# Performance work log

Measured on AMD Instinct MI355X. Metric: run time of the kernel, lower is better.

## Reference

```python
import jax, jax.numpy as jnp
import numpy as np

N, E, FIN, H, C = 100000, 1600000, 128, 64, 40
EPS = 1e-5

def setup_inputs() -> dict:
    key = jax.random.key(0)
    ks = jax.random.split(key, 20)
    inp = {
        'x': jax.random.normal(ks[0], (N, FIN), jnp.float32),
        'edge_idx': jax.random.randint(ks[1], (2, E), 0, N, dtype=jnp.int64),
        'W1': jax.random.normal(ks[2], (FIN, H), jnp.float32) / np.sqrt(FIN),
        'b1': jnp.zeros((H,), jnp.float32),
        'g1': jnp.ones((H,), jnp.float32),
        'be1': jnp.zeros((H,), jnp.float32),
        'm1': jax.random.normal(ks[3], (H,), jnp.float32) * 0.1,
        'v1': jax.random.uniform(ks[4], (H,), jnp.float32) + 0.5,
        'W2': jax.random.normal(ks[5], (H, H), jnp.float32) / np.sqrt(H),
        'b2': jnp.zeros((H,), jnp.float32),
        'g2': jnp.ones((H,), jnp.float32),
        'be2': jnp.zeros((H,), jnp.float32),
        'm2': jax.random.normal(ks[6], (H,), jnp.float32) * 0.1,
        'v2': jax.random.uniform(ks[7], (H,), jnp.float32) + 0.5,
        'W3': jax.random.normal(ks[8], (H, C), jnp.float32) / np.sqrt(H),
        'b3': jnp.zeros((C,), jnp.float32),
    }
    return inp

def reference(x, edge_idx, W1, b1, g1, be1, m1, v1, W2, b2, g2, be2, m2, v2, W3, b3):
    n = x.shape[0]
    loop = jnp.arange(n, dtype=edge_idx.dtype)
    row = jnp.concatenate([edge_idx[0], loop])  # source nodes (+ self loops)
    col = jnp.concatenate([edge_idx[1], loop])  # target nodes (+ self loops)
    # symmetric gcn_norm: deg from unit edge weights aggregated at target
    deg = jax.ops.segment_sum(jnp.ones_like(row, dtype=x.dtype), col, num_segments=n)
    dinv = jnp.where(deg > 0, jax.lax.rsqrt(deg), 0.0)
    norm = dinv[row] * dinv[col]  # [E+N]

    def conv(h, W, b):
        hl = h @ W                            # dense transform first (PyG order)
        msg = hl[row] * norm[:, None]         # gather + edge scale
        agg = jax.ops.segment_sum(msg, col, num_segments=n)  # scatter-add
        return agg + b

    def bn(h, g, be, m, v):  # eval-mode BatchNorm1d (running stats)
        return g * (h - m) * jax.lax.rsqrt(v + EPS) + be

    h = jax.nn.relu(bn(conv(x, W1, b1), g1, be1, m1, v1))
    h = jax.nn.relu(bn(conv(h, W2, b2), g2, be2, m2, v2))
    return conv(h, W3, b3)
```

## Files before the change

### kernel.cpp

```cpp
#include <hip/hip_runtime.h>

#define EPSV 1e-5f
#define NB  1024
#define CAP 2048
#define BIN_ITER 4

typedef short short8 __attribute__((ext_vector_type(8)));
typedef float f32x4 __attribute__((ext_vector_type(4)));

__device__ inline unsigned short f2bf(float x) {
    unsigned u = __float_as_uint(x);
    unsigned r = (u + 0x7FFFu + ((u >> 16) & 1u)) >> 16;
    return (unsigned short)r;
}
__device__ inline float bf2f(unsigned short h) {
    return __uint_as_float(((unsigned)h) << 16);
}
__device__ inline float bflo(unsigned u) { return __uint_as_float(u << 16); }
__device__ inline float bfhi(unsigned u) { return __uint_as_float(u & 0xffff0000u); }
__device__ inline unsigned packbf(float x, float y) {
    return (unsigned)f2bf(x) | ((unsigned)f2bf(y) << 16);
}


__global__ __launch_bounds__(1024) void k_bin(const int* __restrict__ row,
                                              const int* __restrict__ col,
                                              int* __restrict__ bcnt,
                                              unsigned* __restrict__ bkt,
                                              int E, int npb) {
    __shared__ int hist[NB];
    __shared__ int fill[NB];
    const int tid = threadIdx.x;
    const int e0 = blockIdx.x * (1024 * BIN_ITER);
    for (int j = tid; j < NB; j += 1024) hist[j] = 0;
    __syncthreads();
    unsigned ent[BIN_ITER];
    int bb[BIN_ITER];
#pragma unroll
    for (int j = 0; j < BIN_ITER; ++j) {
        const int i = e0 + j * 1024 + tid;
        bb[j] = -1;
        ent[j] = 0;
        if (i < E) {
            const int c = col[i], r = row[i];
            const int b = c / npb;
            bb[j] = b;
            ent[j] = ((unsigned)(c - b * npb) << 17) | (unsigned)r;
            atomicAdd(&hist[b], 1);
        }
    }
    __syncthreads();
    for (int j = tid; j < NB; j += 1024)
        fill[j] = hist[j] ? atomicAdd(&bcnt[j], hist[j]) : 0;
    __syncthreads();
#pragma unroll
    for (int j = 0; j < BIN_ITER; ++j) {
        if (bb[j] >= 0) {
            const int pos = atomicAdd(&fill[bb[j]], 1);
            if (pos < CAP)
                bkt[(size_t)bb[j] * CAP + pos] = ent[j];
        }
    }
}


__global__ __launch_bounds__(NB) void k_bscan(const int* __restrict__ bcnt,
                                              int* __restrict__ bbase,
                                              int* __restrict__ rowptr, int E, int n) {
    __shared__ int s[NB];
    const int t = threadIdx.x;
    const int v = min(bcnt[t], CAP);
    s[t] = v;
    __syncthreads();
    for (int off = 1; off < NB; off <<= 1) {
        int u = (t >= off) ? s[t - off] : 0;
        __syncthreads();
        s[t] += u;
        __syncthreads();
    }
    bbase[t] = s[t] - v;
    if (t == 0) rowptr[n] = E;
}


__global__ __launch_bounds__(256) void k_place(const int* __restrict__ bcnt,
                                               const int* __restrict__ bbase,
                                               const unsigned* __restrict__ bkt,
                                               int* __restrict__ rowptr,
                                               float* __restrict__ dinv,
                                               int* __restrict__ srcidx,
                                               int n, int npb) {
    __shared__ int hist[128];
    __shared__ int pfx[128];
    __shared__ unsigned ent[CAP];
    const int b = blockIdx.x;
    const int tid = threadIdx.x;
    const int c0 = b * npb;
    const int nn = min(npb, n - c0);
    if (nn <= 0) return;
    const int bc = min(bcnt[b], CAP);
    const int base = bbase[b];
    for (int j = tid; j < nn; j += 256) hist[j] = 0;
    __syncthreads();
    for (int i = tid; i < bc; i += 256) {
        const unsigned e = bkt[(size_t)b * CAP + i];
        ent[i] = e;
        atomicAdd(&hist[e >> 17], 1);
    }
    __syncthreads();
    if (tid == 0) {
        int run = base;
        for (int j = 0; j < nn; ++j) { pfx[j] = run; run += hist[j]; }
    }
    __syncthreads();
    for (int j = tid; j < nn; j += 256) {
        rowptr[c0 + j] = pfx[j];
        dinv[c0 + j] = rsqrtf((float)(hist[j] + 1));
    }
    __syncthreads();
    for (int i = tid; i < bc; i += 256) {
        const unsigned e = ent[i];
        const int pos = atomicAdd(&pfx[e >> 17], 1);
        srcidx[pos] = (int)(e & 0x1FFFFu);
    }
}


template<int K, int F, int NT>
__device__ inline void wprep_one(const float* __restrict__ W,
                                 unsigned short* __restrict__ out, int tid) {
    const int lane = tid & 63;
    const int nt = (tid >> 6) % NT;
    const int ks = tid / (64 * NT);
    const int col = nt * 16 + (lane & 15);
    const int k0 = ks * 32 + (lane >> 4) * 8;
    short8 h8, l8;
#pragma unroll
    for (int e = 0; e < 8; ++e) {
        const float w = (col < F) ? W[(size_t)(k0 + e) * F + col] : 0.f;
        const unsigned short h = f2bf(w);
        h8[e] = (short)h;
        l8[e] = (short)f2bf(w - bf2f(h));
    }
    short8* dst = (short8*)(out + (size_t)tid * 16);
    dst[0] = h8;
    dst[1] = l8;
}

__global__ __launch_bounds__(256) void k_wprep_all(const float* __restrict__ W1,
                                                   const float* __restrict__ W2,
                                                   const float* __restrict__ W3,
                                                   unsigned short* __restrict__ wf1,
                                                   unsigned short* __restrict__ wf2,
                                                   unsigned short* __restrict__ wf3) {
    const int tid = blockIdx.x * blockDim.x + threadIdx.x;
    if (tid < 1024) wprep_one<128, 64, 4>(W1, wf1, tid);
    else if (tid < 1536) wprep_one<64, 64, 4>(W2, wf2, tid - 1024);
    else if (tid < 1920) wprep_one<64, 40, 3>(W3, wf3, tid - 1536);
}


template<int K, int NT>
__global__ __launch_bounds__(256) void gemm_f32in(const float* __restrict__ X,
                                                  const unsigned short* __restrict__ wfrag,
                                                  const float* __restrict__ dinv,
                                                  unsigned* __restrict__ Y, int n) {
    const int lane = threadIdx.x & 63;
    const int wv = threadIdx.x >> 6;
    const int row0 = blockIdx.x * 64 + wv * 16;
    const int arow = row0 + (lane & 15);
    const bool aval = arow < n;

    f32x4 acc[NT];
#pragma unroll
    for (int t = 0; t < NT; ++t) acc[t] = (f32x4){0.f, 0.f, 0.f, 0.f};

#pragma unroll
    for (int ks = 0; ks < K / 32; ++ks) {
        float av[8];
        if (aval) {
            const float* ap = X + (size_t)arow * K + ks * 32 + (lane >> 4) * 8;
            const float4 p0 = *reinterpret_cast<const float4*>(ap);
            const float4 p1 = *reinterpret_cast<const float4*>(ap + 4);
            av[0] = p0.x; av[1] = p0.y; av[2] = p0.z; av[3] = p0.w;
            av[4] = p1.x; av[5] = p1.y; av[6] = p1.z; av[7] = p1.w;
        } else {
#pragma unroll
            for (int e = 0; e < 8; ++e) av[e] = 0.f;
        }
        short8 ah, al;
#pragma unroll
        for (int e = 0; e < 8; ++e) {
            const unsigned short h = f2bf(av[e]);
            ah[e] = (short)h;
            al[e] = (short)f2bf(av[e] - bf2f(h));
        }
#pragma unroll
        for (int t = 0; t < NT; ++t) {
            const short8* bp = (const short8*)(wfrag + (((size_t)ks * NT + t) * 64 + lane) * 16);
            const short8 bh = bp[0];
            const short8 bl = bp[1];
            acc[t] = __builtin_amdgcn_mfma_f32_16x16x32_bf16(ah, bh, acc[t], 0, 0, 0);
            acc[t] = __builtin_amdgcn_mfma_f32_16x16x32_bf16(al, bh, acc[t], 0, 0, 0);
            acc[t] = __builtin_amdgcn_mfma_f32_16x16x32_bf16(ah, bl, acc[t], 0, 0, 0);
        }
    }

    const int col = lane & 15;
    const int rg = lane >> 4;
#pragma unroll
    for (int r = 0; r < 4; ++r) {
        const int orow = row0 + rg * 4 + r;
        const float di = (orow < n) ? dinv[orow] : 0.f;
#pragma unroll
        for (int t = 0; t < NT; ++t) {
            const float val = acc[t][r] * di;
            const float oth = __shfl_xor(val, 1);
            if (!(lane & 1))
                Y[(size_t)orow * (NT * 8) + t * 8 + (col >> 1)] = packbf(val, oth);
        }
    }
}


template<int K, int NT, int MODE>
__global__ __launch_bounds__(256) void gemm_bf16in(const unsigned short* __restrict__ X,
                                                   const unsigned short* __restrict__ wfrag,
                                                   const float* __restrict__ dinv,
                                                   const float* __restrict__ bias,
                                                   void* __restrict__ Yv, int n) {
    const int lane = threadIdx.x & 63;
    const int wv = threadIdx.x >> 6;
    const int row0 = blockIdx.x * 64 + wv * 16;
    const int arow = row0 + (lane & 15);
    const bool aval = arow < n;

    f32x4 acc[NT];
#pragma unroll
    for (int t = 0; t < NT; ++t) acc[t] = (f32x4){0.f, 0.f, 0.f, 0.f};

#pragma unroll
    for (int ks = 0; ks < K / 32; ++ks) {
        short8 ah = {0, 0, 0, 0, 0, 0, 0, 0};
        if (aval)
            ah = *(const short8*)(X + (size_t)arow * K + ks * 32 + (lane >> 4) * 8);
#pragma unroll
        for (int t = 0; t < NT; ++t) {
            const short8* bp = (const short8*)(wfrag + (((size_t)ks * NT + t) * 64 + lane) * 16);
            const short8 bh = bp[0];
            const short8 bl = bp[1];
            acc[t] = __builtin_amdgcn_mfma_f32_16x16x32_bf16(ah, bh, acc[t], 0, 0, 0);
            acc[t] = __builtin_amdgcn_mfma_f32_16x16x32_bf16(ah, bl, acc[t], 0, 0, 0);
        }
    }

    const int col = lane & 15;
    const int rg = lane >> 4;
#pragma unroll
    for (int r = 0; r < 4; ++r) {
        const int orow = row0 + rg * 4 + r;
        if (MODE == 0) {
            const float di = (orow < n) ? dinv[orow] : 0.f;
            unsigned* Y = (unsigned*)Yv;
#pragma unroll
            for (int t = 0; t < NT; ++t) {
                const float val = acc[t][r] * di;
                const float oth = __shfl_xor(val, 1);
                if (!(lane & 1))
                    Y[(size_t)orow * (NT * 8) + t * 8 + (col >> 1)] = packbf(val, oth);
            }
        } else {
            float* Y = (float*)Yv;
#pragma unroll
            for (int t = 0; t < NT; ++t) {
                const int oc = t * 16 + col;
                if (orow < n && oc < 40)
                    Y[(size_t)orow * 40 + oc] = acc[t][r] + bias[oc];
            }
        }
    }
}


template<int MODE>
__global__ __launch_bounds__(256) void k_gather(const unsigned* __restrict__ in,
                                                const int* __restrict__ rowptr,
                                                const int* __restrict__ srcidx,
                                                const float* __restrict__ dinv,
                                                const float* __restrict__ b,
                                                const float* __restrict__ g,
                                                const float* __restrict__ be,
                                                const float* __restrict__ m,
                                                const float* __restrict__ v,
                                                unsigned* __restrict__ out, int n) {
    __shared__ unsigned offs[4][64];
    const int lane = threadIdx.x & 63;
    const int wslot = threadIdx.x >> 6;
    const int half = lane >> 5;
    const int p = lane & 31;
    const int node = blockIdx.x * 4 + wslot;

    if (node >= n) {
        if (!half) out[(size_t)node * 32 + p] = 0u;
        return;
    }

    const int s = rowptr[node], e = rowptr[node + 1];
    const unsigned pconst = (unsigned)p * 4u;
    const char* inb = (const char*)in;
    float ax = 0.f, ay = 0.f;

    for (int base = s; base < e; base += 64) {
        const int c = min(64, e - base);
        unsigned idx = (unsigned)n;
        if (base + lane < e) idx = (unsigned)srcidx[base + lane];
        offs[wslot][lane] = idx * 128u;
        for (int k8 = 0; k8 < 32; k8 += 8) {
            if (2 * k8 >= c) break;
            unsigned o[8], u[8];
#pragma unroll
            for (int j = 0; j < 8; ++j) o[j] = offs[wslot][2 * (k8 + j) + half];
#pragma unroll
            for (int j = 0; j < 8; ++j)
                u[j] = *(const unsigned*)(inb + (size_t)(o[j] + pconst));
#pragma unroll
            for (int j = 0; j < 8; ++j) { ax += bflo(u[j]); ay += bfhi(u[j]); }
        }
    }
    ax += __shfl_xor(ax, 32);
    ay += __shfl_xor(ay, 32);
    {
        const unsigned su = in[(size_t)node * 32 + p];
        ax += bflo(su); ay += bfhi(su);
    }
    const float di = dinv[node];
    float ox, oy;
    if (MODE == 2) {
        ox = ax * di; oy = ay * di;
    } else {
        const float2 bb = ((const float2*)b)[p];
        const float2 gg = ((const float2*)g)[p];
        const float2 bee = ((const float2*)be)[p];
        const float2 mm = ((const float2*)m)[p];
        const float2 vv = ((const float2*)v)[p];
        const float sx = gg.x * rsqrtf(vv.x + EPSV);
        const float sy = gg.y * rsqrtf(vv.y + EPSV);
        ox = fmaxf((ax * di + bb.x - mm.x) * sx + bee.x, 0.f);
        oy = fmaxf((ay * di + bb.y - mm.y) * sy + bee.y, 0.f);
        if (MODE == 1) { ox *= di; oy *= di; }
    }
    if (!half) out[(size_t)node * 32 + p] = packbf(ox, oy);
}


extern "C" void kernel_launch(void* const* d_in, const int* in_sizes, int n_in,
                              void* d_out, int out_size, void* d_ws, size_t ws_size,
                              hipStream_t stream) {
    const float* x   = (const float*)d_in[0];
    const int*   ei  = (const int*)d_in[1];
    const float* W1  = (const float*)d_in[2];
    const float* b1  = (const float*)d_in[3];
    const float* g1  = (const float*)d_in[4];
    const float* be1 = (const float*)d_in[5];
    const float* m1  = (const float*)d_in[6];
    const float* v1  = (const float*)d_in[7];
    const float* W2  = (const float*)d_in[8];
    const float* b2  = (const float*)d_in[9];
    const float* g2  = (const float*)d_in[10];
    const float* be2 = (const float*)d_in[11];
    const float* m2  = (const float*)d_in[12];
    const float* v2  = (const float*)d_in[13];
    const float* W3  = (const float*)d_in[14];
    const float* b3  = (const float*)d_in[15];

    const int n = in_sizes[0] / 128;
    const int E = in_sizes[1] / 2;
    const int* row  = ei;
    const int* colv = ei + E;
    const int npb = (n + NB - 1) / NB;
    const int gblk = (n >> 6) + 1;
    const int npad = gblk * 64;

    char* base = (char*)d_ws;
    size_t off = 0;
    auto alloc = [&](size_t bytes) -> char* {
        char* p = base + off;
        off += (bytes + 255) & ~(size_t)255;
        return p;
    };
    int*      bcnt   = (int*)     alloc((size_t)NB * 4);
    int*      bbase  = (int*)     alloc((size_t)NB * 4);
    unsigned* bkt    = (unsigned*)alloc((size_t)NB * CAP * 4);
    int*      rowptr = (int*)     alloc((size_t)(n + 1) * 4);
    int*      srcidx = (int*)     alloc((size_t)E * 4);
    float*    dinv   = (float*)   alloc((size_t)n * 4);
    unsigned* hls1u  = (unsigned*)alloc((size_t)npad * 32 * 4);
    unsigned* h1u    = (unsigned*)alloc((size_t)npad * 32 * 4);
    unsigned* hls2u  = (unsigned*)alloc((size_t)npad * 32 * 4);
    unsigned* h2lsu  = (unsigned*)alloc((size_t)npad * 32 * 4);
    unsigned* agg3u  = (unsigned*)alloc((size_t)npad * 32 * 4);
    unsigned short* wf1 = (unsigned short*)alloc((size_t)(128/32) * 4 * 64 * 32);
    unsigned short* wf2 = (unsigned short*)alloc((size_t)(64/32) * 4 * 64 * 32);
    unsigned short* wf3 = (unsigned short*)alloc((size_t)(64/32) * 3 * 64 * 32);
    float*    outp   = (float*)d_out;

    hipMemsetAsync(bcnt, 0, (size_t)NB * 4, stream);
    const int binblk = (E + 1024 * BIN_ITER - 1) / (1024 * BIN_ITER);
    k_bin<<<binblk, 1024, 0, stream>>>(row, colv, bcnt, bkt, E, npb);
    k_bscan<<<1, NB, 0, stream>>>(bcnt, bbase, rowptr, E, n);
    k_place<<<NB, 256, 0, stream>>>(bcnt, bbase, bkt, rowptr, dinv, srcidx, n, npb);

    k_wprep_all<<<8, 256, 0, stream>>>(W1, W2, W3, wf1, wf2, wf3);

    const int ablk = npad / 4;
    gemm_f32in<128, 4><<<gblk, 256, 0, stream>>>(x, wf1, dinv, hls1u, n);
    k_gather<0><<<ablk, 256, 0, stream>>>(hls1u, rowptr, srcidx, dinv,
                                          b1, g1, be1, m1, v1, h1u, n);
    gemm_bf16in<64, 4, 0><<<gblk, 256, 0, stream>>>((const unsigned short*)h1u, wf2,
                                                    dinv, nullptr, hls2u, n);
    k_gather<1><<<ablk, 256, 0, stream>>>(hls2u, rowptr, srcidx, dinv,
                                          b2, g2, be2, m2, v2, h2lsu, n);
    k_gather<2><<<ablk, 256, 0, stream>>>(h2lsu, rowptr, srcidx, dinv,
                                          nullptr, nullptr, nullptr, nullptr, nullptr,
                                          agg3u, n);
    gemm_bf16in<64, 3, 1><<<gblk, 256, 0, stream>>>((const unsigned short*)agg3u, wf3,
                                                    dinv, b3, outp, n);
}
```

Measured before the change: 196.0 us.

## Process eight nodes per wavefront in CSR gather, drop LDS index staging

The gather kernel now assigns eight consecutive nodes to each wavefront instead of one. Row pointers are loaded once per wave and broadcast with readlane, and the BatchNorm parameters are hoisted out of the per-node loop. Neighbor indices are read directly from global memory in groups of 16 rather than staged through shared memory, which removes LDS traffic and per-node launch overhead. The cost is fewer waves in flight for latency hiding, and the 16-edge granularity wastes lanes on low-degree nodes.

Measured after the change: 201.9 us. 3.0% more time.

```diff
diff --git a/kernel.cpp b/kernel.cpp
--- a/kernel.cpp
+++ b/kernel.cpp
@@ -292,64 +292,71 @@
                                                 const float* __restrict__ be,
                                                 const float* __restrict__ m,
                                                 const float* __restrict__ v,
-                                                unsigned* __restrict__ out, int n) {
-    __shared__ unsigned offs[4][64];
+                                                unsigned* __restrict__ out,
+                                                int n, int E) {
     const int lane = threadIdx.x & 63;
-    const int wslot = threadIdx.x >> 6;
     const int half = lane >> 5;
     const int p = lane & 31;
-    const int node = blockIdx.x * 4 + wslot;
-
-    if (node >= n) {
-        if (!half) out[(size_t)node * 32 + p] = 0u;
-        return;
-    }
-
-    const int s = rowptr[node], e = rowptr[node + 1];
-    const unsigned pconst = (unsigned)p * 4u;
-    const char* inb = (const char*)in;
-    float ax = 0.f, ay = 0.f;
-
-    for (int base = s; base < e; base += 64) {
-        const int c = min(64, e - base);
-        unsigned idx = (unsigned)n;
-        if (base + lane < e) idx = (unsigned)srcidx[base + lane];
-        offs[wslot][lane] = idx * 128u;
-        for (int k8 = 0; k8 < 32; k8 += 8) {
-            if (2 * k8 >= c) break;
-            unsigned o[8], u[8];
-#pragma unroll
-            for (int j = 0; j < 8; ++j) o[j] = offs[wslot][2 * (k8 + j) + half];
-#pragma unroll
-            for (int j = 0; j < 8; ++j)
-                u[j] = *(const unsigned*)(inb + (size_t)(o[j] + pconst));
+    int node0 = (blockIdx.x * 4 + (threadIdx.x >> 6)) * 8;
+    node0 = __builtin_amdgcn_readfirstlane(node0);
+
+    const int rp = rowptr[min(node0 + min(lane, 8), n)];
+
+    float sx = 0.f, sy = 0.f;
+    float2 bb = {0.f, 0.f}, mm = {0.f, 0.f}, bee = {0.f, 0.f};
+    if (MODE != 2) {
+        bb = ((const float2*)b)[p];
+        const float2 gg = ((const float2*)g)[p];
+        bee = ((const float2*)be)[p];
+        mm = ((const float2*)m)[p];
+        const float2 vv = ((const float2*)v)[p];
+        sx = gg.x * rsqrtf(vv.x + EPSV);
+        sy = gg.y * rsqrtf(vv.y + EPSV);
+    }
+
+    for (int i = 0; i < 8; ++i) {
+        const int node = node0 + i;
+        if (node >= n) {
+            if (!half) out[(size_t)node * 32 + p] = 0u;
+            continue;
+        }
+        const int s = __builtin_amdgcn_readlane(rp, i);
+        const int e = __builtin_amdgcn_readlane(rp, i + 1);
+        float ax = 0.f, ay = 0.f;
+        for (int gb = s; gb < e; gb += 16) {
+            int idxv[8];
+            unsigned u[8];
+#pragma unroll
+            for (int j = 0; j < 8; ++j) {
+                const int pos = gb + 2 * j + half;
+                idxv[j] = srcidx[min(pos, E - 1)];
+            }
+#pragma unroll
+            for (int j = 0; j < 8; ++j) {
+                const int pos = gb + 2 * j + half;
+                const unsigned rowi = (pos < e) ? (unsigned)idxv[j] : (unsigned)n;
+                u[j] = in[(size_t)rowi * 32 + p];
+            }
 #pragma unroll
             for (int j = 0; j < 8; ++j) { ax += bflo(u[j]); ay += bfhi(u[j]); }
         }
-    }
-    ax += __shfl_xor(ax, 32);
-    ay += __shfl_xor(ay, 32);
-    {
-        const unsigned su = in[(size_t)node * 32 + p];
-        ax += bflo(su); ay += bfhi(su);
-    }
-    const float di = dinv[node];
-    float ox, oy;
-    if (MODE == 2) {
-        ox = ax * di; oy = ay * di;
-    } else {
-        const float2 bb = ((const float2*)b)[p];
-        const float2 gg = ((const float2*)g)[p];
-        const float2 bee = ((const float2*)be)[p];
-        const float2 mm = ((const float2*)m)[p];
-        const float2 vv = ((const float2*)v)[p];
-        const float sx = gg.x * rsqrtf(vv.x + EPSV);
-        const float sy = gg.y * rsqrtf(vv.y + EPSV);
-        ox = fmaxf((ax * di + bb.x - mm.x) * sx + bee.x, 0.f);
-        oy = fmaxf((ay * di + bb.y - mm.y) * sy + bee.y, 0.f);
-        if (MODE == 1) { ox *= di; oy *= di; }
-    }
-    if (!half) out[(size_t)node * 32 + p] = packbf(ox, oy);
+        ax += __shfl_xor(ax, 32);
+        ay += __shfl_xor(ay, 32);
+        {
+            const unsigned su = in[(size_t)node * 32 + p];
+            ax += bflo(su); ay += bfhi(su);
+        }
+        const float di = dinv[node];
+        float ox, oy;
+        if (MODE == 2) {
+            ox = ax * di; oy = ay * di;
+        } else {
+            ox = fmaxf((ax * di + bb.x - mm.x) * sx + bee.x, 0.f);
+            oy = fmaxf((ay * di + bb.y - mm.y) * sy + bee.y, 0.f);
+            if (MODE == 1) { ox *= di; oy *= di; }
+        }
+        if (!half) out[(size_t)node * 32 + p] = packbf(ox, oy);
+    }
 }
 
 
@@ -412,17 +419,17 @@
 
     k_wprep_all<<<8, 256, 0, stream>>>(W1, W2, W3, wf1, wf2, wf3);
 
-    const int ablk = npad / 4;
+    const int ablk = (npad / 8 + 3) / 4;
     gemm_f32in<128, 4><<<gblk, 256, 0, stream>>>(x, wf1, dinv, hls1u, n);
     k_gather<0><<<ablk, 256, 0, stream>>>(hls1u, rowptr, srcidx, dinv,
-                                          b1, g1, be1, m1, v1, h1u, n);
+                                          b1, g1, be1, m1, v1, h1u, n, E);
     gemm_bf16in<64, 4, 0><<<gblk, 256, 0, stream>>>((const unsigned short*)h1u, wf2,
                                                     dinv, nullptr, hls2u, n);
     k_gather<1><<<ablk, 256, 0, stream>>>(hls2u, rowptr, srcidx, dinv,
-                                          b2, g2, be2, m2, v2, h2lsu, n);
+                                          b2, g2, be2, m2, v2, h2lsu, n, E);
     k_gather<2><<<ablk, 256, 0, stream>>>(h2lsu, rowptr, srcidx, dinv,
                                           nullptr, nullptr, nullptr, nullptr, nullptr,
-                                          agg3u, n);
+                                          agg3u, n, E);
     gemm_bf16in<64, 3, 1><<<gblk, 256, 0, stream>>>((const unsigned short*)agg3u, wf3,
                                                     dinv, b3, outp, n);
 }
```
